# Optimization experiments

Hardware: AMD Instinct MI355X
Metric: run time of the kernel (lower is better)

## Reference

```python
import jax, jax.numpy as jnp
import numpy as np

E = 100000          # number of edges
IN_FEATS = 256      # in_edge_feats
HIDDEN = 128        # hidden_size
K = 16              # neighbors per edge (uniform-degree rendering of ragged lists)


def setup_inputs() -> dict:
    key = jax.random.key(0)
    k1, k2, k3, k4 = jax.random.split(key, 4)
    edge_feats = jax.random.normal(k1, (E, IN_FEATS), dtype=jnp.float32)
    neighbors = jax.random.randint(k2, (E, K), 0, E, dtype=jnp.int32)
    # Linear params (torch Linear: y = x @ W^T + b; here W stored as [in, out])
    W = jax.random.normal(k3, (IN_FEATS, HIDDEN), dtype=jnp.float32) / np.sqrt(IN_FEATS)
    b = jax.random.normal(k4, (HIDDEN,), dtype=jnp.float32) * 0.01
    return {"edge_feats": edge_feats, "neighbors": neighbors, "W": W, "b": b}


def reference(edge_feats, neighbors, W, b):
    # Dense linear transform of all edge features: [E, H]
    t = edge_feats @ W + b
    # Gather each edge's K neighbor transformed features and sum: [E, K, H] -> [E, H]
    nbr_sum = jnp.take(t, neighbors, axis=0).sum(axis=1)
    # agg[i] = t[i] + sum_{n in neighbors[i]} t[n]
    return t + nbr_sum
```

## Files before the change

kernel.cpp:

```cpp
#include <hip/hip_runtime.h>
#include <hip/hip_bf16.h>
#include <stdint.h>

#define E_EDGES 100000
#define IN_F    256
#define HID     128
#define KNB     16

typedef short bf16x8 __attribute__((ext_vector_type(8)));
typedef float f32x4  __attribute__((ext_vector_type(4)));

__device__ __forceinline__ unsigned short f2bf(float f) {
    union { float f; unsigned u; } v; v.f = f;
    unsigned u = v.u;
    u += 0x7fffu + ((u >> 16) & 1u);
    return (unsigned short)(u >> 16);
}

__global__ void conv_w_kernel(const float* __restrict__ W, unsigned short* __restrict__ Wt) {
    int t = blockIdx.x * blockDim.x + threadIdx.x;
    int n = t & (HID - 1);
    int k = t >> 7;
    Wt[(size_t)n * IN_F + k] = f2bf(W[(size_t)k * HID + n]);
}

__launch_bounds__(256)
__global__ void conv_a_kernel(const float* __restrict__ A, unsigned short* __restrict__ Abf) {
    size_t i = ((size_t)blockIdx.x * 256 + threadIdx.x) * 8;
    float4 lo = *(const float4*)(A + i);
    float4 hi = *(const float4*)(A + i + 4);
    uint4 o;
    o.x = (unsigned)f2bf(lo.x) | ((unsigned)f2bf(lo.y) << 16);
    o.y = (unsigned)f2bf(lo.z) | ((unsigned)f2bf(lo.w) << 16);
    o.z = (unsigned)f2bf(hi.x) | ((unsigned)f2bf(hi.y) << 16);
    o.w = (unsigned)f2bf(hi.z) | ((unsigned)f2bf(hi.w) << 16);
    *(uint4*)(Abf + i) = o;
}

__launch_bounds__(256)
__global__ void gemm_t_kernel(const unsigned short* __restrict__ Abf,
                              const unsigned short* __restrict__ Wt,
                              const float* __restrict__ bias,
                              unsigned short* __restrict__ T) {
    __shared__ unsigned short Bs[32768];
    const int tid = threadIdx.x;

    #pragma unroll
    for (int it = 0; it < 16; ++it) {
        int e    = it * 256 + tid;
        int n    = e >> 5;
        int k8   = e & 31;
        int dst  = ((k8 >> 2) * 8 + (n >> 4)) * 64 + (k8 & 3) * 16 + (n & 15);
        uint4 v = *(const uint4*)(Wt + (size_t)e * 8);
        *(uint4*)(Bs + (size_t)dst * 8) = v;
    }

    const int wave = tid >> 6;
    const int lane = tid & 63;
    const int l15  = lane & 15;
    const int quad = lane >> 4;
    const int rowbase = blockIdx.x * 64 + wave * 16;
    int arow = rowbase + l15;
    if (arow >= E_EDGES) arow = E_EDGES - 1;

    const unsigned short* ap = Abf + (size_t)arow * IN_F + quad * 8;
    bf16x8 apre[8];
    #pragma unroll
    for (int k0 = 0; k0 < 8; ++k0)
        apre[k0] = *(const bf16x8*)(ap + k0 * 32);

    __syncthreads();

    f32x4 acc[8] = {};
    #pragma unroll
    for (int k0 = 0; k0 < 8; ++k0) {
        #pragma unroll
        for (int ct = 0; ct < 8; ++ct) {
            bf16x8 bf = *(const bf16x8*)(Bs + ((size_t)((k0 * 8 + ct) * 64 + lane)) * 8);
            acc[ct] = __builtin_amdgcn_mfma_f32_16x16x32_bf16(apre[k0], bf, acc[ct], 0, 0, 0);
        }
    }

    #pragma unroll
    for (int ct = 0; ct < 8; ++ct) {
        const int col = ct * 16 + l15;
        const float bv = bias[col];
        #pragma unroll
        for (int i = 0; i < 4; ++i) {
            const int row = rowbase + quad * 4 + i;
            if (row < E_EDGES)
                T[(size_t)row * HID + col] = f2bf(acc[ct][i] + bv);
        }
    }
}

__launch_bounds__(256)
__global__ void gather_sum_kernel(const unsigned short* __restrict__ T,
                                  const int* __restrict__ nbr,
                                  float* __restrict__ out) {
    __shared__ int sidx[256];
    const int tid   = threadIdx.x;
    const int edge0 = blockIdx.x * 16;
    sidx[tid] = nbr[(size_t)edge0 * KNB + tid];
    __syncthreads();

    const int el   = tid >> 4;
    const int lane = tid & 15;
    const int edge = edge0 + el;

    float acc[8];
    {
        uint4 v = *(const uint4*)(T + (size_t)edge * HID + lane * 8);
        unsigned w[4] = { v.x, v.y, v.z, v.w };
        union { unsigned u; float f; } c;
        #pragma unroll
        for (int j = 0; j < 4; ++j) {
            c.u = w[j] << 16;          acc[2 * j]     = c.f;
            c.u = w[j] & 0xffff0000u;  acc[2 * j + 1] = c.f;
        }
    }
    #pragma unroll
    for (int k = 0; k < KNB; ++k) {
        const int n = sidx[el * KNB + k];
        uint4 v = *(const uint4*)(T + (size_t)n * HID + lane * 8);
        unsigned w[4] = { v.x, v.y, v.z, v.w };
        union { unsigned u; float f; } c;
        #pragma unroll
        for (int j = 0; j < 4; ++j) {
            c.u = w[j] << 16;          acc[2 * j]     += c.f;
            c.u = w[j] & 0xffff0000u;  acc[2 * j + 1] += c.f;
        }
    }

    float* op = out + (size_t)edge * HID + lane * 8;
    float4 o0 = { acc[0], acc[1], acc[2], acc[3] };
    float4 o1 = { acc[4], acc[5], acc[6], acc[7] };
    *(float4*)op       = o0;
    *(float4*)(op + 4) = o1;
}

extern "C" void kernel_launch(void* const* d_in, const int* in_sizes, int n_in,
                              void* d_out, int out_size, void* d_ws, size_t ws_size,
                              hipStream_t stream) {
    const float* edge_feats = (const float*)d_in[0];
    const int*   neighbors  = (const int*)d_in[1];
    const float* W          = (const float*)d_in[2];
    const float* b          = (const float*)d_in[3];
    float*       out        = (float*)d_out;

    unsigned short* Wt  = (unsigned short*)d_ws;
    unsigned short* T   = (unsigned short*)d_ws + (size_t)IN_F * HID;
    unsigned short* Abf = (unsigned short*)d_out;

    conv_w_kernel<<<(IN_F * HID) / 256, 256, 0, stream>>>(W, Wt);
    conv_a_kernel<<<(E_EDGES * IN_F) / (256 * 8), 256, 0, stream>>>(edge_feats, Abf);
    gemm_t_kernel<<<(E_EDGES + 63) / 64, 256, 0, stream>>>(Abf, Wt, b, T);
    gather_sum_kernel<<<E_EDGES / 16, 256, 0, stream>>>(T, neighbors, out);
}
```

Before: 264.3 us.

## Fuse fp32-to-bf16 conversion of edge features into GEMM kernel

```diff
diff --git a/kernel.cpp b/kernel.cpp
--- a/kernel.cpp
+++ b/kernel.cpp
@@ -25,25 +25,27 @@
 }
 
 __launch_bounds__(256)
-__global__ void conv_a_kernel(const float* __restrict__ A, unsigned short* __restrict__ Abf) {
-    size_t i = ((size_t)blockIdx.x * 256 + threadIdx.x) * 8;
-    float4 lo = *(const float4*)(A + i);
-    float4 hi = *(const float4*)(A + i + 4);
-    uint4 o;
-    o.x = (unsigned)f2bf(lo.x) | ((unsigned)f2bf(lo.y) << 16);
-    o.y = (unsigned)f2bf(lo.z) | ((unsigned)f2bf(lo.w) << 16);
-    o.z = (unsigned)f2bf(hi.x) | ((unsigned)f2bf(hi.y) << 16);
-    o.w = (unsigned)f2bf(hi.z) | ((unsigned)f2bf(hi.w) << 16);
-    *(uint4*)(Abf + i) = o;
-}
-
-__launch_bounds__(256)
-__global__ void gemm_t_kernel(const unsigned short* __restrict__ Abf,
+__global__ void gemm_t_kernel(const float* __restrict__ A,
                               const unsigned short* __restrict__ Wt,
                               const float* __restrict__ bias,
                               unsigned short* __restrict__ T) {
     __shared__ unsigned short Bs[32768];
-    const int tid = threadIdx.x;
+    const int tid  = threadIdx.x;
+    const int wave = tid >> 6;
+    const int lane = tid & 63;
+    const int l15  = lane & 15;
+    const int quad = lane >> 4;
+    const int rowbase = blockIdx.x * 64 + wave * 16;
+    int arow = rowbase + l15;
+    if (arow >= E_EDGES) arow = E_EDGES - 1;
+
+    const float* ap = A + (size_t)arow * IN_F + quad * 8;
+    float4 af32[16];
+    #pragma unroll
+    for (int k0 = 0; k0 < 8; ++k0) {
+        af32[2 * k0]     = *(const float4*)(ap + k0 * 32);
+        af32[2 * k0 + 1] = *(const float4*)(ap + k0 * 32 + 4);
+    }
 
     #pragma unroll
     for (int it = 0; it < 16; ++it) {
@@ -54,22 +56,19 @@
         uint4 v = *(const uint4*)(Wt + (size_t)e * 8);
         *(uint4*)(Bs + (size_t)dst * 8) = v;
     }
+    __syncthreads();
 
-    const int wave = tid >> 6;
-    const int lane = tid & 63;
-    const int l15  = lane & 15;
-    const int quad = lane >> 4;
-    const int rowbase = blockIdx.x * 64 + wave * 16;
-    int arow = rowbase + l15;
-    if (arow >= E_EDGES) arow = E_EDGES - 1;
-
-    const unsigned short* ap = Abf + (size_t)arow * IN_F + quad * 8;
     bf16x8 apre[8];
     #pragma unroll
-    for (int k0 = 0; k0 < 8; ++k0)
-        apre[k0] = *(const bf16x8*)(ap + k0 * 32);
-
-    __syncthreads();
+    for (int k0 = 0; k0 < 8; ++k0) {
+        float4 lo = af32[2 * k0], hi = af32[2 * k0 + 1];
+        bf16x8 f;
+        f[0] = (short)f2bf(lo.x); f[1] = (short)f2bf(lo.y);
+        f[2] = (short)f2bf(lo.z); f[3] = (short)f2bf(lo.w);
+        f[4] = (short)f2bf(hi.x); f[5] = (short)f2bf(hi.y);
+        f[6] = (short)f2bf(hi.z); f[7] = (short)f2bf(hi.w);
+        apre[k0] = f;
+    }
 
     f32x4 acc[8] = {};
     #pragma unroll
@@ -133,10 +132,10 @@
     }
 
     float* op = out + (size_t)edge * HID + lane * 8;
-    float4 o0 = { acc[0], acc[1], acc[2], acc[3] };
-    float4 o1 = { acc[4], acc[5], acc[6], acc[7] };
-    *(float4*)op       = o0;
-    *(float4*)(op + 4) = o1;
+    f32x4 o0 = { acc[0], acc[1], acc[2], acc[3] };
+    f32x4 o1 = { acc[4], acc[5], acc[6], acc[7] };
+    __builtin_nontemporal_store(o0, (f32x4*)op);
+    __builtin_nontemporal_store(o1, (f32x4*)(op + 4));
 }
 
 extern "C" void kernel_launch(void* const* d_in, const int* in_sizes, int n_in,
@@ -148,12 +147,10 @@
     const float* b          = (const float*)d_in[3];
     float*       out        = (float*)d_out;
 
-    unsigned short* Wt  = (unsigned short*)d_ws;
-    unsigned short* T   = (unsigned short*)d_ws + (size_t)IN_F * HID;
-    unsigned short* Abf = (unsigned short*)d_out;
+    unsigned short* Wt = (unsigned short*)d_ws;
+    unsigned short* T  = (unsigned short*)d_ws + (size_t)IN_F * HID;
 
     conv_w_kernel<<<(IN_F * HID) / 256, 256, 0, stream>>>(W, Wt);
-    conv_a_kernel<<<(E_EDGES * IN_F) / (256 * 8), 256, 0, stream>>>(edge_feats, Abf);
-    gemm_t_kernel<<<(E_EDGES + 63) / 64, 256, 0, stream>>>(Abf, Wt, b, T);
+    gemm_t_kernel<<<(E_EDGES + 63) / 64, 256, 0, stream>>>(edge_feats, Wt, b, T);
     gather_sum_kernel<<<E_EDGES / 16, 256, 0, stream>>>(T, neighbors, out);
 }
```

Result: faster. 245.7 us (-7.0%).
